# Kernel optimization log

Measured on AMD Instinct MI355X. Metric: run time of the kernel, lower is better.

Reference implementation:

```python
import jax, jax.numpy as jnp
import numpy as np

B, S, D, F, E = 8, 2048, 768, 3072, 8


def setup_inputs() -> dict:
    key = jax.random.key(0)
    k1, k2, k3, k4 = jax.random.split(key, 4)
    return {
        "hidden_states": jax.random.normal(k1, (B, S, D), dtype=jnp.float32),
        "router_w": jax.random.normal(k2, (D, E), dtype=jnp.float32) * 0.02,
        "w_in": jax.random.normal(k3, (E, D, F), dtype=jnp.float32) * 0.02,
        "w_out": jax.random.normal(k4, (E, F, D), dtype=jnp.float32) * 0.02,
    }


def reference(hidden_states, router_w, w_in, w_out):
    b, s, d = hidden_states.shape
    x = hidden_states.reshape(-1, d)                    # [T, D] tokens
    router_logits = x @ router_w                        # [T, E]
    router_probs_full = jax.nn.softmax(router_logits, axis=-1)
    expert_index = jnp.argmax(router_probs_full, axis=-1)          # top-1 routing
    onehot = jax.nn.one_hot(expert_index, E, dtype=x.dtype)        # [T, E] router_mask
    top_prob = jnp.max(router_probs_full, axis=-1, keepdims=True)  # [T, 1] router_probs

    # Per-expert FFN (relu MLP); every token is processed by exactly one expert,
    # expert outputs overwrite the token (gather/scatter combine in the original).
    y = jnp.zeros_like(x)
    for e in range(E):  # fixed small expert count; weights structurally distinct
        h = jax.nn.relu(x @ w_in[e]) @ w_out[e]
        y = y + onehot[:, e:e + 1] * h

    out = (top_prob * y).reshape(b, s, d)
    return out, router_logits, expert_index
```

## Files before the change

kernel.cpp:

```cpp
#include <hip/hip_runtime.h>
#include <hip/hip_bf16.h>

constexpr int T  = 16384;
constexpr int Dh = 768;
constexpr int Fh = 3072;
constexpr int Eh = 8;
constexpr int MAXT2 = T / 256 + Eh;

typedef unsigned short ushort_t;
typedef __attribute__((ext_vector_type(8))) short  bf16x8;
typedef __attribute__((ext_vector_type(4))) float  f32x4;

static __device__ __forceinline__ ushort_t f2bf(float f) {
    unsigned u = __builtin_bit_cast(unsigned, f);
    u += 0x7FFFu + ((u >> 16) & 1u);
    return (ushort_t)(u >> 16);
}

__global__ __launch_bounds__(1024) void router_kernel(
    const float* __restrict__ x, const float* __restrict__ rw,
    float* __restrict__ logits_out, float* __restrict__ eidx_out,
    float* __restrict__ topp, int* __restrict__ counts, int* __restrict__ perm) {

    __shared__ float rwT[Eh][Dh];
    __shared__ int   sAmax[16];
    __shared__ int   sBase[Eh];

    int tid = threadIdx.x;
    for (int i = tid; i < Dh * Eh; i += 1024) {
        int d = i >> 3, e = i & 7;
        rwT[e][d] = rw[i];
    }
    __syncthreads();

    int wave = tid >> 6, lane = tid & 63;
    int t = blockIdx.x * 16 + wave;
    const float* xr = x + (size_t)t * Dh;

    double acc[Eh];
#pragma unroll
    for (int e = 0; e < Eh; ++e) acc[e] = 0.0;

#pragma unroll
    for (int j = 0; j < Dh / 256; ++j) {
        int d = lane * 4 + j * 256;
        const float4 xv = *(const float4*)(xr + d);
#pragma unroll
        for (int e = 0; e < Eh; ++e) {
            const float4 w = *(const float4*)&rwT[e][d];
            acc[e] += (double)xv.x * (double)w.x + (double)xv.y * (double)w.y
                    + (double)xv.z * (double)w.z + (double)xv.w * (double)w.w;
        }
    }
#pragma unroll
    for (int off = 32; off > 0; off >>= 1) {
#pragma unroll
        for (int e = 0; e < Eh; ++e) acc[e] += __shfl_xor(acc[e], off, 64);
    }

    int amax = 0;
    if (lane == 0) {
        float l32[Eh];
        float m = -3.4e38f;
#pragma unroll
        for (int e = 0; e < Eh; ++e) l32[e] = (float)acc[e];
#pragma unroll
        for (int e = 0; e < Eh; ++e) {
            if (l32[e] > m) { m = l32[e]; amax = e; }
        }
        float s = 0.f;
#pragma unroll
        for (int e = 0; e < Eh; ++e) s += expf(l32[e] - m);
#pragma unroll
        for (int e = 0; e < Eh; ++e) logits_out[(size_t)t * Eh + e] = l32[e];
        eidx_out[t] = (float)amax;
        topp[t]     = 1.0f / s;
        sAmax[wave] = amax;
    }
    __syncthreads();

    if (tid < Eh) {
        int c = 0;
#pragma unroll
        for (int w = 0; w < 16; ++w) c += (sAmax[w] == tid);
        sBase[tid] = (c > 0) ? atomicAdd(&counts[tid], c) : 0;
    }
    __syncthreads();

    if (lane == 0) {
        int prior = 0;
        for (int w = 0; w < wave; ++w) prior += (sAmax[w] == amax);
        perm[amax * T + sBase[amax] + prior] = t;
    }
}

__global__ void scan_counts(const int* counts, int* offsets,
                            int* tE, int* tGoff, int* tSlot0, int* tRows, int* nT) {
    int lane = threadIdx.x;
    if (lane < Eh) {
        int coff = 0, toff = 0;
        for (int e = 0; e < lane; ++e) {
            int ce = counts[e];
            coff += ce;
            toff += (ce + 255) >> 8;
        }
        int c = counts[lane];
        offsets[lane] = coff;
        int myt = (c + 255) >> 8;
        for (int k = 0; k < myt; ++k) {
            int idx = toff + k;
            tE[idx]     = lane;
            tGoff[idx]  = coff + k * 256;
            tSlot0[idx] = k * 256;
            int rem = c - k * 256;
            tRows[idx]  = rem < 256 ? rem : 256;
        }
        if (lane == Eh - 1) {
            offsets[Eh] = coff + c;
            nT[0] = toff + myt;
        }
    }
}

__global__ void gather_cast_x(const float* __restrict__ x, const int* __restrict__ offsets,
                              const int* __restrict__ perm, ushort_t* __restrict__ Xg) {
    __shared__ int soff[Eh + 1];
    if (threadIdx.x < Eh + 1) soff[threadIdx.x] = offsets[threadIdx.x];
    __syncthreads();
    int q  = blockIdx.x * 256 + threadIdx.x;
    int g  = q / (Dh / 4);
    int cq = (q - g * (Dh / 4)) * 4;
    int e = 0;
#pragma unroll
    for (int i = 1; i < Eh; ++i) e += (g >= soff[i]);
    int tok = perm[e * T + (g - soff[e])];
    const float4 v = *(const float4*)(x + (size_t)tok * Dh + cq);
    ushort4 o;
    o.x = f2bf(v.x); o.y = f2bf(v.y); o.z = f2bf(v.z); o.w = f2bf(v.w);
    *(ushort4*)(Xg + (size_t)g * Dh + cq) = o;
}

__global__ __launch_bounds__(256) void transpose_cvt(
    const float* __restrict__ src, ushort_t* __restrict__ dst, int R, int C) {
    __shared__ ushort_t tile[64][65];
    int tid = threadIdx.x;
    size_t base = (size_t)blockIdx.z * (size_t)R * (size_t)C;
    int c0 = blockIdx.x * 64, r0 = blockIdx.y * 64;
    int rr  = tid >> 4;
    int cc4 = (tid & 15) * 4;
#pragma unroll
    for (int p = 0; p < 4; ++p) {
        int r = rr + p * 16;
        const float4 v = *(const float4*)(src + base + (size_t)(r0 + r) * C + c0 + cc4);
        tile[r][cc4 + 0] = f2bf(v.x);
        tile[r][cc4 + 1] = f2bf(v.y);
        tile[r][cc4 + 2] = f2bf(v.z);
        tile[r][cc4 + 3] = f2bf(v.w);
    }
    __syncthreads();
    int co = tid >> 4;
    int rp = (tid & 15) * 4;
#pragma unroll
    for (int p = 0; p < 4; ++p) {
        int c = co + p * 16;
        ushort4 o = { tile[rp][c], tile[rp + 1][c], tile[rp + 2][c], tile[rp + 3][c] };
        *(ushort4*)(dst + base + (size_t)(c0 + c) * R + r0 + rp) = o;
    }
}

template<int KTOT, int NTOT, int MODE>
__global__ __launch_bounds__(512, 2) void moe_gemm2(
    const ushort_t* __restrict__ Aall, const ushort_t* __restrict__ Ball,
    const int* __restrict__ tE, const int* __restrict__ tGoff,
    const int* __restrict__ tSlot0, const int* __restrict__ tRows,
    const int* __restrict__ nT,
    const int* __restrict__ perm, const float* __restrict__ topp,
    void* __restrict__ Cout)
{
    constexpr int NY  = NTOT / 256;
    constexpr int NWG = MAXT2 * NY;
    constexpr int CPX = NWG / 8;

    int hw  = blockIdx.x;
    int wid = (hw & 7) * CPX + (hw >> 3);
    int ytile = wid / MAXT2;
    int i     = wid - ytile * MAXT2;

    if (i >= nT[0]) return;
    int e     = tE[i];
    int goff  = tGoff[i];
    int slot0 = tSlot0[i];
    int rows  = tRows[i];
    int n0    = ytile * 256;

    const ushort_t* Ap = Aall + (size_t)goff * KTOT;
    const ushort_t* Bp = Ball + (size_t)e * KTOT * NTOT + (size_t)n0 * KTOT;

    __shared__ ushort_t As[2][256 * 64];
    __shared__ ushort_t Bs[2][256 * 64];
    __shared__ int   tokLds[256];
    __shared__ float probLds[256];

    int tid = threadIdx.x, lane = tid & 63, wid_w = tid >> 6;
    int wr = wid_w >> 2, wc = wid_w & 3;
    int gq = lane >> 4, lm = lane & 15, l7 = lane & 7;

    if (MODE == 1 && tid < 256) {
        int tok = (tid < rows) ? perm[e * T + slot0 + tid] : 0;
        tokLds[tid]  = tok;
        probLds[tid] = (tid < rows) ? topp[tok] : 0.f;
    }

    f32x4 acc[8][4];
    const f32x4 zero = {0.f, 0.f, 0.f, 0.f};
#pragma unroll
    for (int mi = 0; mi < 8; ++mi)
#pragma unroll
        for (int ni = 0; ni < 4; ++ni) acc[mi][ni] = zero;

    bf16x8 bb0[4], bb1[4];
    bf16x8 afb[2][2];

#define STAGE_A(BUF, KT) { \
    _Pragma("unroll") \
    for (int j = 0; j < 4; ++j) { \
        int c_ = tid + j * 512; \
        int rr = c_ >> 3, gg = c_ & 7; \
        int srow_ = rr < rows ? rr : rows - 1; \
        const ushort_t* src_ = Ap + (size_t)srow_ * KTOT + (size_t)(KT) * 64 + ((gg ^ (rr & 7)) << 3); \
        __builtin_amdgcn_global_load_lds( \
            (const __attribute__((address_space(1))) unsigned int*)src_, \
            (__attribute__((address_space(3))) unsigned int*)&As[BUF][rr * 64 + gg * 8], 16, 0, 0); \
    } }

#define STAGE_B(BUF, KT) { \
    _Pragma("unroll") \
    for (int j = 0; j < 4; ++j) { \
        int c_ = tid + j * 512; \
        int rr = c_ >> 3, gg = c_ & 7; \
        const ushort_t* src_ = Bp + (size_t)rr * KTOT + (size_t)(KT) * 64 + ((gg ^ (rr & 7)) << 3); \
        __builtin_amdgcn_global_load_lds( \
            (const __attribute__((address_space(1))) unsigned int*)src_, \
            (__attribute__((address_space(3))) unsigned int*)&Bs[BUF][rr * 64 + gg * 8], 16, 0, 0); \
    } }

#define READ_B_KS(TB_, KS, DST) { \
    _Pragma("unroll") \
    for (int ni = 0; ni < 4; ++ni) \
        DST[ni] = *(const bf16x8*)&Bs[TB_][ \
            (wc * 64 + ni * 16 + lm) * 64 + (((((KS) << 2) + gq) ^ l7) << 3)]; \
    }

#define READ_A_MI(TB_, MI, DST) { \
    _Pragma("unroll") \
    for (int ks = 0; ks < 2; ++ks) \
        DST[ks] = *(const bf16x8*)&As[TB_][ \
            (wr * 128 + (MI) * 16 + lm) * 64 + ((((ks << 2) + gq) ^ l7) << 3)]; \
    }

#define MFMA_KS(MI, SRC, KS, BB) { \
    __builtin_amdgcn_s_setprio(1); \
    _Pragma("unroll") \
    for (int ni = 0; ni < 4; ++ni) \
        acc[MI][ni] = __builtin_amdgcn_mfma_f32_16x16x32_bf16( \
            SRC[KS], BB[ni], acc[MI][ni], 0, 0, 0); \
    __builtin_amdgcn_s_setprio(0); }

    const int nkt = KTOT / 64;

    STAGE_A(0, 0);
    STAGE_B(0, 0);
    if (nkt > 1) {
        STAGE_B(1, 1);
        asm volatile("s_waitcnt vmcnt(4)" ::: "memory");
    } else {
        asm volatile("s_waitcnt vmcnt(0)" ::: "memory");
    }
    __builtin_amdgcn_sched_barrier(0);
    __builtin_amdgcn_s_barrier();
    READ_B_KS(0, 0, bb0);
    READ_B_KS(0, 1, bb1);
    READ_A_MI(0, 0, afb[0]);

    for (int t = 0; t < nkt; ++t) {
        const int TB = t & 1;

        if (t + 1 < nkt) STAGE_A(TB ^ 1, t + 1);
        asm volatile("s_waitcnt lgkmcnt(0)" ::: "memory");
        __builtin_amdgcn_sched_barrier(0);
        __builtin_amdgcn_s_barrier();
        if (t + 2 < nkt) STAGE_B(TB, t + 2);

#pragma unroll
        for (int mi = 0; mi < 7; ++mi) {
            READ_A_MI(TB, mi + 1, afb[(mi + 1) & 1]);
            MFMA_KS(mi, afb[mi & 1], 0, bb0);
            MFMA_KS(mi, afb[mi & 1], 1, bb1);
        }

        if (t + 1 < nkt) {
            if (t + 2 < nkt) {
                asm volatile("s_waitcnt vmcnt(4)" ::: "memory");
            } else {
                asm volatile("s_waitcnt vmcnt(0)" ::: "memory");
            }
            __builtin_amdgcn_sched_barrier(0);
            READ_A_MI(TB ^ 1, 0, afb[0]);
            MFMA_KS(7, afb[1], 0, bb0);
            READ_B_KS(TB ^ 1, 0, bb0);
            MFMA_KS(7, afb[1], 1, bb1);
            READ_B_KS(TB ^ 1, 1, bb1);
        } else {
            MFMA_KS(7, afb[1], 0, bb0);
            MFMA_KS(7, afb[1], 1, bb1);
        }
        __builtin_amdgcn_s_barrier();
    }

    int cr = (lane >> 4) * 4;
    int cc = lane & 15;
#pragma unroll
    for (int mi = 0; mi < 8; ++mi) {
#pragma unroll
        for (int r = 0; r < 4; ++r) {
            int m = wr * 128 + mi * 16 + cr + r;
            if (m < rows) {
                if (MODE == 0) {
                    ushort_t* hp = (ushort_t*)Cout + (size_t)(goff + m) * NTOT
                                 + n0 + wc * 64 + cc;
#pragma unroll
                    for (int ni = 0; ni < 4; ++ni) {
                        float v = acc[mi][ni][r];
                        hp[ni * 16] = f2bf(v > 0.f ? v : 0.f);
                    }
                } else {
                    int tok = tokLds[m];
                    float p = probLds[m];
                    float* op = (float*)Cout + (size_t)tok * NTOT
                              + n0 + wc * 64 + cc;
#pragma unroll
                    for (int ni = 0; ni < 4; ++ni) op[ni * 16] = acc[mi][ni][r] * p;
                }
            }
        }
    }
#undef STAGE_A
#undef STAGE_B
#undef READ_B_KS
#undef READ_A_MI
#undef MFMA_KS
}

constexpr size_t OFF_COUNTS  = 0;
constexpr size_t OFF_OFFSETS = 256;
constexpr size_t OFF_TILES   = 512;
constexpr size_t OFF_TOPP    = OFF_TILES + 4 * 144 * 5 + 64;
constexpr size_t OFF_PERM    = OFF_TOPP + (size_t)T * 4;
constexpr size_t OFF_XG      = (OFF_PERM + (size_t)Eh * T * 4 + 255) & ~(size_t)255;
constexpr size_t OFF_H       = (OFF_XG + (size_t)(T + 128) * Dh * 2 + 255) & ~(size_t)255;
constexpr size_t OFF_WIN     = (OFF_H + (size_t)(T + 128) * Fh * 2 + 255) & ~(size_t)255;
constexpr size_t OFF_WOUT    = (OFF_WIN + (size_t)Eh * Dh * Fh * 2 + 255) & ~(size_t)255;

extern "C" void kernel_launch(void* const* d_in, const int* in_sizes, int n_in,
                              void* d_out, int out_size, void* d_ws, size_t ws_size,
                              hipStream_t stream) {
    const float* x    = (const float*)d_in[0];
    const float* rw   = (const float*)d_in[1];
    const float* w_in = (const float*)d_in[2];
    const float* w_out= (const float*)d_in[3];

    float* out    = (float*)d_out;
    float* logits = out + (size_t)T * Dh;
    float* eidx   = logits + (size_t)T * Eh;

    char* ws = (char*)d_ws;
    int*      counts  = (int*)(ws + OFF_COUNTS);
    int*      offsets = (int*)(ws + OFF_OFFSETS);
    int*      tE      = (int*)(ws + OFF_TILES);
    int*      tGoff   = tE + 144;
    int*      tSlot0  = tGoff + 144;
    int*      tRows   = tSlot0 + 144;
    int*      nT      = tRows + 144;
    float*    topp    = (float*)(ws + OFF_TOPP);
    int*      perm    = (int*)(ws + OFF_PERM);
    ushort_t* Xg      = (ushort_t*)(ws + OFF_XG);
    ushort_t* h       = (ushort_t*)(ws + OFF_H);
    ushort_t* WinT    = (ushort_t*)(ws + OFF_WIN);
    ushort_t* WoutT   = (ushort_t*)(ws + OFF_WOUT);

    hipMemsetAsync(counts, 0, Eh * sizeof(int), stream);
    router_kernel<<<T / 16, 1024, 0, stream>>>(x, rw, logits, eidx, topp, counts, perm);
    scan_counts<<<1, 64, 0, stream>>>(counts, offsets, tE, tGoff, tSlot0, tRows, nT);
    gather_cast_x<<<(T * (Dh / 4)) / 256, 256, 0, stream>>>(x, offsets, perm, Xg);
    transpose_cvt<<<dim3(Fh / 64, Dh / 64, Eh), 256, 0, stream>>>(w_in, WinT, Dh, Fh);
    transpose_cvt<<<dim3(Dh / 64, Fh / 64, Eh), 256, 0, stream>>>(w_out, WoutT, Fh, Dh);
    moe_gemm2<Dh, Fh, 0><<<dim3(MAXT2 * (Fh / 256)), 512, 0, stream>>>(
        Xg, WinT, tE, tGoff, tSlot0, tRows, nT, perm, topp, (void*)h);
    moe_gemm2<Fh, Dh, 1><<<dim3(MAXT2 * (Dh / 256)), 512, 0, stream>>>(
        h, WoutT, tE, tGoff, tSlot0, tRows, nT, perm, topp, (void*)out);
}
```

Baseline: 510.7 us.

## Switch MoE GEMM to four-stage K=32 pipeline and reorder XCD tile mapping

The grouped expert GEMM now stages K in slices of 32 across a 4-slot LDS ring, prefetching three slices ahead, where it previously used double-buffered K=64 tiles with interleaved register prefetch. Each iteration loads all A and B fragments and then issues 32 MFMAs. Block-to-tile mapping now assigns 9 consecutive row tiles per XCD across all column tiles, aiming for L2 reuse of expert weights and activations. Risks: one barrier per 32-K slice doubles sync count, LDS reads no longer overlap MFMAs within the iteration, and the hardcoded 9 only covers all row tiles if MAXT2 is at most 72.

```diff
diff --git a/kernel.cpp b/kernel.cpp
--- a/kernel.cpp
+++ b/kernel.cpp
@@ -177,14 +177,10 @@
     const int* __restrict__ perm, const float* __restrict__ topp,
     void* __restrict__ Cout)
 {
-    constexpr int NY  = NTOT / 256;
-    constexpr int NWG = MAXT2 * NY;
-    constexpr int CPX = NWG / 8;
-
-    int hw  = blockIdx.x;
-    int wid = (hw & 7) * CPX + (hw >> 3);
-    int ytile = wid / MAXT2;
-    int i     = wid - ytile * MAXT2;
+    int xcd = blockIdx.x & 7;
+    int pos = blockIdx.x >> 3;
+    int ytile = pos / 9;
+    int i     = xcd * 9 + (pos - ytile * 9);
 
     if (i >= nT[0]) return;
     int e     = tE[i];
@@ -196,14 +192,15 @@
     const ushort_t* Ap = Aall + (size_t)goff * KTOT;
     const ushort_t* Bp = Ball + (size_t)e * KTOT * NTOT + (size_t)n0 * KTOT;
 
-    __shared__ ushort_t As[2][256 * 64];
-    __shared__ ushort_t Bs[2][256 * 64];
+    __shared__ ushort_t As[4][256 * 32];
+    __shared__ ushort_t Bs[4][256 * 32];
     __shared__ int   tokLds[256];
     __shared__ float probLds[256];
 
     int tid = threadIdx.x, lane = tid & 63, wid_w = tid >> 6;
     int wr = wid_w >> 2, wc = wid_w & 3;
-    int gq = lane >> 4, lm = lane & 15, l7 = lane & 7;
+    int gq = lane >> 4, lm = lane & 15;
+    int lm3 = lm & 3;
 
     if (MODE == 1 && tid < 256) {
         int tok = (tid < rows) ? perm[e * T + slot0 + tid] : 0;
@@ -218,101 +215,66 @@
 #pragma unroll
         for (int ni = 0; ni < 4; ++ni) acc[mi][ni] = zero;
 
-    bf16x8 bb0[4], bb1[4];
-    bf16x8 afb[2][2];
-
-#define STAGE_A(BUF, KT) { \
+#define STAGE(SLOT, KT) { \
     _Pragma("unroll") \
-    for (int j = 0; j < 4; ++j) { \
+    for (int j = 0; j < 2; ++j) { \
         int c_ = tid + j * 512; \
-        int rr = c_ >> 3, gg = c_ & 7; \
+        int rr = c_ >> 2, gg = c_ & 3; \
         int srow_ = rr < rows ? rr : rows - 1; \
-        const ushort_t* src_ = Ap + (size_t)srow_ * KTOT + (size_t)(KT) * 64 + ((gg ^ (rr & 7)) << 3); \
+        const ushort_t* srcA_ = Ap + (size_t)srow_ * KTOT + (size_t)(KT) * 32 + ((gg ^ (rr & 3)) << 3); \
         __builtin_amdgcn_global_load_lds( \
-            (const __attribute__((address_space(1))) unsigned int*)src_, \
-            (__attribute__((address_space(3))) unsigned int*)&As[BUF][rr * 64 + gg * 8], 16, 0, 0); \
+            (const __attribute__((address_space(1))) unsigned int*)srcA_, \
+            (__attribute__((address_space(3))) unsigned int*)&As[SLOT][c_ * 8], 16, 0, 0); \
+    } \
+    _Pragma("unroll") \
+    for (int j = 0; j < 2; ++j) { \
+        int c_ = tid + j * 512; \
+        int rr = c_ >> 2, gg = c_ & 3; \
+        const ushort_t* srcB_ = Bp + (size_t)rr * KTOT + (size_t)(KT) * 32 + ((gg ^ (rr & 3)) << 3); \
+        __builtin_amdgcn_global_load_lds( \
+            (const __attribute__((address_space(1))) unsigned int*)srcB_, \
+            (__attribute__((address_space(3))) unsigned int*)&Bs[SLOT][c_ * 8], 16, 0, 0); \
     } }
 
-#define STAGE_B(BUF, KT) { \
-    _Pragma("unroll") \
-    for (int j = 0; j < 4; ++j) { \
-        int c_ = tid + j * 512; \
-        int rr = c_ >> 3, gg = c_ & 7; \
-        const ushort_t* src_ = Bp + (size_t)rr * KTOT + (size_t)(KT) * 64 + ((gg ^ (rr & 7)) << 3); \
-        __builtin_amdgcn_global_load_lds( \
-            (const __attribute__((address_space(1))) unsigned int*)src_, \
-            (__attribute__((address_space(3))) unsigned int*)&Bs[BUF][rr * 64 + gg * 8], 16, 0, 0); \
-    } }
-
-#define READ_B_KS(TB_, KS, DST) { \
-    _Pragma("unroll") \
-    for (int ni = 0; ni < 4; ++ni) \
-        DST[ni] = *(const bf16x8*)&Bs[TB_][ \
-            (wc * 64 + ni * 16 + lm) * 64 + (((((KS) << 2) + gq) ^ l7) << 3)]; \
-    }
-
-#define READ_A_MI(TB_, MI, DST) { \
-    _Pragma("unroll") \
-    for (int ks = 0; ks < 2; ++ks) \
-        DST[ks] = *(const bf16x8*)&As[TB_][ \
-            (wr * 128 + (MI) * 16 + lm) * 64 + ((((ks << 2) + gq) ^ l7) << 3)]; \
-    }
-
-#define MFMA_KS(MI, SRC, KS, BB) { \
-    __builtin_amdgcn_s_setprio(1); \
-    _Pragma("unroll") \
-    for (int ni = 0; ni < 4; ++ni) \
-        acc[MI][ni] = __builtin_amdgcn_mfma_f32_16x16x32_bf16( \
-            SRC[KS], BB[ni], acc[MI][ni], 0, 0, 0); \
-    __builtin_amdgcn_s_setprio(0); }
-
-    const int nkt = KTOT / 64;
-
-    STAGE_A(0, 0);
-    STAGE_B(0, 0);
-    if (nkt > 1) {
-        STAGE_B(1, 1);
-        asm volatile("s_waitcnt vmcnt(4)" ::: "memory");
-    } else {
-        asm volatile("s_waitcnt vmcnt(0)" ::: "memory");
-    }
+    const int nkt = KTOT / 32;
+
+    STAGE(0, 0);
+    STAGE(1, 1);
+    STAGE(2, 2);
+    asm volatile("s_waitcnt vmcnt(8)" ::: "memory");
     __builtin_amdgcn_sched_barrier(0);
     __builtin_amdgcn_s_barrier();
-    READ_B_KS(0, 0, bb0);
-    READ_B_KS(0, 1, bb1);
-    READ_A_MI(0, 0, afb[0]);
 
     for (int t = 0; t < nkt; ++t) {
-        const int TB = t & 1;
-
-        if (t + 1 < nkt) STAGE_A(TB ^ 1, t + 1);
-        asm volatile("s_waitcnt lgkmcnt(0)" ::: "memory");
-        __builtin_amdgcn_sched_barrier(0);
-        __builtin_amdgcn_s_barrier();
-        if (t + 2 < nkt) STAGE_B(TB, t + 2);
-
-#pragma unroll
-        for (int mi = 0; mi < 7; ++mi) {
-            READ_A_MI(TB, mi + 1, afb[(mi + 1) & 1]);
-            MFMA_KS(mi, afb[mi & 1], 0, bb0);
-            MFMA_KS(mi, afb[mi & 1], 1, bb1);
-        }
+        const int SL = t & 3;
+        if (t + 3 < nkt) STAGE((t + 3) & 3, t + 3);
+
+        bf16x8 af[8], bb[4];
+#pragma unroll
+        for (int ni = 0; ni < 4; ++ni)
+            bb[ni] = *(const bf16x8*)&Bs[SL][(wc * 64 + ni * 16 + lm) * 32 + ((gq ^ lm3) << 3)];
+#pragma unroll
+        for (int mi = 0; mi < 8; ++mi)
+            af[mi] = *(const bf16x8*)&As[SL][(wr * 128 + mi * 16 + lm) * 32 + ((gq ^ lm3) << 3)];
+
+        __builtin_amdgcn_s_setprio(1);
+#pragma unroll
+        for (int mi = 0; mi < 8; ++mi)
+#pragma unroll
+            for (int ni = 0; ni < 4; ++ni)
+                acc[mi][ni] = __builtin_amdgcn_mfma_f32_16x16x32_bf16(
+                    af[mi], bb[ni], acc[mi][ni], 0, 0, 0);
+        __builtin_amdgcn_s_setprio(0);
 
         if (t + 1 < nkt) {
-            if (t + 2 < nkt) {
+            if (t + 3 < nkt) {
+                asm volatile("s_waitcnt vmcnt(8)" ::: "memory");
+            } else if (t + 2 < nkt) {
                 asm volatile("s_waitcnt vmcnt(4)" ::: "memory");
             } else {
                 asm volatile("s_waitcnt vmcnt(0)" ::: "memory");
             }
             __builtin_amdgcn_sched_barrier(0);
-            READ_A_MI(TB ^ 1, 0, afb[0]);
-            MFMA_KS(7, afb[1], 0, bb0);
-            READ_B_KS(TB ^ 1, 0, bb0);
-            MFMA_KS(7, afb[1], 1, bb1);
-            READ_B_KS(TB ^ 1, 1, bb1);
-        } else {
-            MFMA_KS(7, afb[1], 0, bb0);
-            MFMA_KS(7, afb[1], 1, bb1);
         }
         __builtin_amdgcn_s_barrier();
     }
@@ -344,11 +306,7 @@
             }
         }
     }
-#undef STAGE_A
-#undef STAGE_B
-#undef READ_B_KS
-#undef READ_A_MI
-#undef MFMA_KS
+#undef STAGE
 }
 
 constexpr size_t OFF_COUNTS  = 0;
```

New measurement: 532.6 us. +4.3%, slower.
